# Optimization experiments

Hardware: AMD Instinct MI355X
Metric: run time of the kernel (lower is better)

Reference implementation:

```python
import jax, jax.numpy as jnp
import numpy as np

ALPHA = 0.2  # LeakyReLU negative slope
NEG_INF = -9e15


def setup_inputs() -> dict:
    key = jax.random.key(0)
    k1, k2, k3, k4, k5 = jax.random.split(key, 5)
    B, N, D = 4, 4096, 256
    feat = jax.random.normal(k1, (B, N, D), dtype=jnp.float32)
    adj = jax.random.randint(k2, (B, N, N), 0, 2, dtype=jnp.int32)
    W = jax.random.normal(k3, (D, D), dtype=jnp.float32) * (1.414 / np.sqrt(D))
    a_1 = jax.random.normal(k4, (D, 1), dtype=jnp.float32) * 0.1
    a_2 = jax.random.normal(k5, (D, 1), dtype=jnp.float32) * 0.1
    return {"feat": feat, "adj": adj, "W": W, "a_1": a_1, "a_2": a_2}


def reference(feat, adj, W, a_1, a_2):
    # h: [B, N, D]
    h = jnp.matmul(feat, W)
    Ax = jnp.matmul(h, a_1)  # [B, N, 1]
    Ay = jnp.matmul(h, a_2)  # [B, N, 1]
    # logits[b, i, j] = Ax[b, j] + Ay[b, i]
    logits = jnp.swapaxes(Ax, 1, 2) + Ay  # [B, N, N]
    e = jax.nn.leaky_relu(logits, negative_slope=ALPHA)
    e = jnp.where(adj > 0, e, jnp.float32(NEG_INF))
    attention = jax.nn.softmax(e, axis=-1)  # dropout p=0.0 -> identity
    h_prime = jnp.matmul(attention, feat)  # [B, N, in_features]
    h_out = jnp.matmul(h_prime, W)  # [B, N, out_features]
    return jax.nn.elu(h_out)
```

## Files before the change

### kernel.cpp

```cpp
#include <hip/hip_runtime.h>

typedef __attribute__((ext_vector_type(8))) short short8;
typedef __attribute__((ext_vector_type(4))) float f32x4;

#define LOG2E 1.44269504f

__device__ __forceinline__ short f2bf(float f) {
  unsigned u = __builtin_bit_cast(unsigned, f);
  u += 0x7fffu + ((u >> 16) & 1u);
  return (short)(u >> 16);
}

__global__ void gat_wvec(const float* __restrict__ W, const float* __restrict__ a1,
                         const float* __restrict__ a2, float* __restrict__ w1,
                         float* __restrict__ w2) {
  __shared__ float a1f[256], a2f[256];
  const int tid = threadIdx.x;
  a1f[tid] = a1[tid];
  a2f[tid] = a2[tid];
  __syncthreads();
  float s1 = 0.f, s2 = 0.f;
  const float4* wr = (const float4*)(W + (size_t)tid * 256);
  for (int d0 = 0; d0 < 64; ++d0) {
    float4 v = wr[d0];
    s1 += v.x * a1f[d0 * 4] + v.y * a1f[d0 * 4 + 1] + v.z * a1f[d0 * 4 + 2] + v.w * a1f[d0 * 4 + 3];
    s2 += v.x * a2f[d0 * 4] + v.y * a2f[d0 * 4 + 1] + v.z * a2f[d0 * 4 + 2] + v.w * a2f[d0 * 4 + 3];
  }
  w1[tid] = s1;
  w2[tid] = s2;
}

__global__ void convT(const float* __restrict__ src, short* __restrict__ dst,
                      int R, int C) {
  __shared__ short T[64][72];
  const int tid = threadIdx.x;
  const int bc = blockIdx.x, br = blockIdx.y, bb = blockIdx.z;
  const float* s = src + (size_t)bb * R * C;
  short* d = dst + (size_t)bb * R * C;
  const int rr = tid >> 2, cc = (tid & 3) << 4;
  const float4* sp = (const float4*)(s + (size_t)(br * 64 + rr) * C + bc * 64 + cc);
  alignas(16) short v[16];
#pragma unroll
  for (int g = 0; g < 4; ++g) {
    float4 x = sp[g];
    v[g * 4 + 0] = f2bf(x.x);
    v[g * 4 + 1] = f2bf(x.y);
    v[g * 4 + 2] = f2bf(x.z);
    v[g * 4 + 3] = f2bf(x.w);
  }
  *(short8*)&T[rr][cc] = *(short8*)&v[0];
  *(short8*)&T[rr][cc + 8] = *(short8*)&v[8];
  __syncthreads();
#pragma unroll
  for (int j = 0; j < 16; ++j) v[j] = T[cc + j][rr];
  short8* dp = (short8*)(d + (size_t)(bc * 64 + rr) * R + br * 64 + cc);
  dp[0] = *(short8*)&v[0];
  dp[1] = *(short8*)&v[8];
}

__global__ void gat_axay(const float* __restrict__ feat, const float* __restrict__ w1,
                         const float* __restrict__ w2, float* __restrict__ Ax,
                         float* __restrict__ Ay) {
  const int lane = threadIdx.x & 63;
  const int row = blockIdx.x * 4 + (threadIdx.x >> 6);
  float4 fv = *(const float4*)(feat + (size_t)row * 256 + lane * 4);
  const float4 w1v = *(const float4*)(w1 + lane * 4);
  const float4 w2v = *(const float4*)(w2 + lane * 4);
  float s1 = fv.x * w1v.x + fv.y * w1v.y + fv.z * w1v.z + fv.w * w1v.w;
  float s2 = fv.x * w2v.x + fv.y * w2v.y + fv.z * w2v.z + fv.w * w2v.w;
#pragma unroll
  for (int off = 32; off >= 1; off >>= 1) {
    s1 += __shfl_xor(s1, off);
    s2 += __shfl_xor(s2, off);
  }
  if (lane == 0) { Ax[row] = s1; Ay[row] = s2; }
}

__global__ void gat_max(const float* __restrict__ Ax, float* __restrict__ Mb) {
  __shared__ float red[256];
  const int b = blockIdx.x, tid = threadIdx.x;
  float m = -3.4e38f;
  for (int i = tid; i < 4096; i += 256) m = fmaxf(m, Ax[b * 4096 + i]);
  red[tid] = m;
  __syncthreads();
  for (int s = 128; s > 0; s >>= 1) {
    if (tid < s) red[tid] = fmaxf(red[tid], red[tid + s]);
    __syncthreads();
  }
  if (tid == 0) Mb[b] = red[0];
}

__global__ __launch_bounds__(256, 2) void gat_attn(
    const short* __restrict__ featT,
    const int* __restrict__ adj,
    const float* __restrict__ Ax, const float* __restrict__ Ay,
    const float* __restrict__ Mb,
    float* __restrict__ Opart,
    float* __restrict__ lpart)
{
  __shared__ short Pbuf[2][64][72];
  __shared__ float lsbuf[256];
  const int tid = threadIdx.x;
  const int blk = blockIdx.x;
  const int s = blk & 1;
  const int it = (blk >> 1) & 63;
  const int b = blk >> 7;
  const int i0 = it << 6;
  const int jbase = s << 11;

  const int r = tid >> 2;
  const int c0 = (tid & 3) << 4;

  const float ay = Ay[b * 4096 + i0 + r];
  float mr = ay + Mb[b];
  mr = mr > 0.f ? mr : 0.2f * mr;

  const int lane = tid & 63;
  const int w = tid >> 6;
  const int n0 = w << 6;
  const int l15 = lane & 15;
  const int q = lane >> 4;

  f32x4 acc[4][4];
#pragma unroll
  for (int i = 0; i < 4; ++i)
#pragma unroll
    for (int j = 0; j < 4; ++j) acc[i][j] = (f32x4){0.f, 0.f, 0.f, 0.f};

  float lsum = 0.f;

  const int4* adjp = (const int4*)(adj + ((size_t)(b * 4096 + i0 + r)) * 4096 + jbase + c0);
  const float4* axp = (const float4*)(Ax + b * 4096 + jbase + c0);
  const short* ftb = featT + ((size_t)(b * 256 + n0 + l15)) * 4096 + jbase + q * 8;

  int4 adv[4];
  float4 axv[4];
#pragma unroll
  for (int g = 0; g < 4; ++g) { adv[g] = adjp[g]; axv[g] = axp[g]; }

  for (int c = 0; c < 32; ++c) {
    alignas(16) short pk[16];
#pragma unroll
    for (int g = 0; g < 4; ++g) {
      const int* ai = (const int*)&adv[g];
      const float* af = (const float*)&axv[g];
#pragma unroll
      for (int u = 0; u < 4; ++u) {
        float lg = af[u] + ay;
        float e = lg > 0.f ? lg : 0.2f * lg;
        e = ai[u] > 0 ? e : -9e15f;
        float p = __builtin_amdgcn_exp2f((e - mr) * LOG2E);
        lsum += p;
        pk[g * 4 + u] = f2bf(p);
      }
    }
    {
      short8* dst = (short8*)&Pbuf[c & 1][r][c0];
      dst[0] = *(short8*)&pk[0];
      dst[1] = *(short8*)&pk[8];
    }
    __syncthreads();

    if (c < 31) {
#pragma unroll
      for (int g = 0; g < 4; ++g) {
        adv[g] = adjp[(c + 1) * 16 + g];
        axv[g] = axp[(c + 1) * 16 + g];
      }
    }

    const int j0 = c << 6;
#pragma unroll
    for (int k0 = 0; k0 < 64; k0 += 32) {
      short8 afr[4];
#pragma unroll
      for (int rt = 0; rt < 4; ++rt)
        afr[rt] = *(const short8*)&Pbuf[c & 1][rt * 16 + l15][k0 + q * 8];
#pragma unroll
      for (int ct = 0; ct < 4; ++ct) {
        short8 bfr = *(const short8*)(ftb + (size_t)ct * 16 * 4096 + j0 + k0);
#pragma unroll
        for (int rt = 0; rt < 4; ++rt)
          acc[rt][ct] = __builtin_amdgcn_mfma_f32_16x16x32_bf16(afr[rt], bfr, acc[rt][ct], 0, 0, 0);
      }
    }
  }

  lsbuf[tid] = lsum;
  __syncthreads();
  if (tid < 64) {
    float t = lsbuf[tid * 4] + lsbuf[tid * 4 + 1] + lsbuf[tid * 4 + 2] + lsbuf[tid * 4 + 3];
    lpart[(size_t)s * 16384 + b * 4096 + i0 + tid] = t;
  }
  float* Od = Opart + (size_t)s * 16384 * 256;
#pragma unroll
  for (int rt = 0; rt < 4; ++rt)
#pragma unroll
    for (int reg = 0; reg < 4; ++reg) {
      int row = i0 + rt * 16 + q * 4 + reg;
      float* orow = Od + ((size_t)(b * 4096 + row)) * 256 + n0 + l15;
#pragma unroll
      for (int ct = 0; ct < 4; ++ct) orow[ct * 16] = acc[rt][ct][reg];
    }
}

__global__ __launch_bounds__(256, 2) void gat_out(
    const float* __restrict__ O,
    const float* __restrict__ lp,
    const short* __restrict__ WT,
    float* __restrict__ out)
{
  const int tid = threadIdx.x;
  const int lane = tid & 63;
  const int w = tid >> 6;
  const int r0 = blockIdx.x << 6;
  const int n0 = w << 6;
  const int l15 = lane & 15;
  const int q = lane >> 4;

  f32x4 acc[4][4];
#pragma unroll
  for (int i = 0; i < 4; ++i)
#pragma unroll
    for (int j = 0; j < 4; ++j) acc[i][j] = (f32x4){0.f, 0.f, 0.f, 0.f};

  float linv[4];
#pragma unroll
  for (int rt = 0; rt < 4; ++rt) {
    int row = r0 + rt * 16 + l15;
    float l = lp[row] + lp[16384 + row];
    linv[rt] = l > 0.f ? 1.f / l : 0.f;
  }
  const float* O2 = O + (size_t)16384 * 256;

#pragma unroll 2
  for (int k0 = 0; k0 < 256; k0 += 32) {
    short8 afr[4];
#pragma unroll
    for (int rt = 0; rt < 4; ++rt) {
      size_t off = (size_t)(r0 + rt * 16 + l15) * 256 + k0 + q * 8;
      f32x4 h0 = *(const f32x4*)(O + off) + *(const f32x4*)(O2 + off);
      f32x4 h1 = *(const f32x4*)(O + off + 4) + *(const f32x4*)(O2 + off + 4);
      h0 *= linv[rt];
      h1 *= linv[rt];
      alignas(16) short p[8];
#pragma unroll
      for (int j = 0; j < 4; ++j) { p[j] = f2bf(h0[j]); p[4 + j] = f2bf(h1[j]); }
      afr[rt] = *(short8*)p;
    }
#pragma unroll
    for (int ct = 0; ct < 4; ++ct) {
      short8 bfr = *(const short8*)(WT + (size_t)(n0 + ct * 16 + l15) * 256 + k0 + q * 8);
#pragma unroll
      for (int rt = 0; rt < 4; ++rt)
        acc[rt][ct] = __builtin_amdgcn_mfma_f32_16x16x32_bf16(afr[rt], bfr, acc[rt][ct], 0, 0, 0);
    }
  }
#pragma unroll
  for (int rt = 0; rt < 4; ++rt)
#pragma unroll
    for (int reg = 0; reg < 4; ++reg) {
      int row = r0 + rt * 16 + q * 4 + reg;
#pragma unroll
      for (int ct = 0; ct < 4; ++ct) {
        float v = acc[rt][ct][reg];
        float o = v > 0.f ? v : (__builtin_amdgcn_exp2f(v * LOG2E) - 1.f);
        out[(size_t)row * 256 + n0 + ct * 16 + l15] = o;
      }
    }
}

extern "C" void kernel_launch(void* const* d_in, const int* in_sizes, int n_in,
                              void* d_out, int out_size, void* d_ws, size_t ws_size,
                              hipStream_t stream) {
  (void)in_sizes; (void)n_in; (void)out_size; (void)ws_size;
  const float* feat = (const float*)d_in[0];
  const int* adj = (const int*)d_in[1];
  const float* W = (const float*)d_in[2];
  const float* a1 = (const float*)d_in[3];
  const float* a2 = (const float*)d_in[4];
  float* out = (float*)d_out;

  char* ws = (char*)d_ws;
  short* featT = (short*)ws;
  float* Opart = (float*)(ws + 8388608);
  short* WT    = (short*)(ws + 41943040);
  float* w1    = (float*)(ws + 42074112);
  float* w2    = (float*)(ws + 42075136);
  float* Ax    = (float*)(ws + 42076160);
  float* Ay    = (float*)(ws + 42141696);
  float* lpart = (float*)(ws + 42207232);
  float* Mb    = (float*)(ws + 42338304);

  hipLaunchKernelGGL(gat_wvec, dim3(1), dim3(256), 0, stream, W, a1, a2, w1, w2);
  hipLaunchKernelGGL(convT, dim3(4, 4, 1), dim3(256), 0, stream, W, WT, 256, 256);
  hipLaunchKernelGGL(convT, dim3(4, 64, 4), dim3(256), 0, stream, feat, featT, 4096, 256);
  hipLaunchKernelGGL(gat_axay, dim3(4096), dim3(256), 0, stream, feat, w1, w2, Ax, Ay);
  hipLaunchKernelGGL(gat_max, dim3(4), dim3(256), 0, stream, Ax, Mb);
  hipLaunchKernelGGL(gat_attn, dim3(512), dim3(256), 0, stream, featT, adj, Ax, Ay, Mb, Opart, lpart);
  hipLaunchKernelGGL(gat_out, dim3(256), dim3(256), 0, stream, Opart, lpart, WT, out);
}
```

Measured before the change: 484.8 us.

## Fuse output projection into attention kernel and drop split-K over columns

```diff
diff --git a/kernel.cpp b/kernel.cpp
--- a/kernel.cpp
+++ b/kernel.cpp
@@ -2,6 +2,7 @@
 
 typedef __attribute__((ext_vector_type(8))) short short8;
 typedef __attribute__((ext_vector_type(4))) float f32x4;
+typedef __attribute__((ext_vector_type(4))) int i32x4;
 
 #define LOG2E 1.44269504f
 
@@ -95,21 +96,22 @@
     const int* __restrict__ adj,
     const float* __restrict__ Ax, const float* __restrict__ Ay,
     const float* __restrict__ Mb,
-    float* __restrict__ Opart,
-    float* __restrict__ lpart)
+    const short* __restrict__ WT,
+    float* __restrict__ out)
 {
-  __shared__ short Pbuf[2][64][72];
-  __shared__ float lsbuf[256];
+  __shared__ short Pbuf[2][32][72];
+  __shared__ short hbuf[32 * 264];
+  __shared__ float linv_s[32];
+
   const int tid = threadIdx.x;
   const int blk = blockIdx.x;
-  const int s = blk & 1;
-  const int it = (blk >> 1) & 63;
-  const int b = blk >> 7;
-  const int i0 = it << 6;
-  const int jbase = s << 11;
-
-  const int r = tid >> 2;
-  const int c0 = (tid & 3) << 4;
+  const int x = blk & 7;
+  const int b = x >> 1;
+  const int it = ((blk >> 3) << 1) | (x & 1);
+  const int i0 = it << 5;
+
+  const int r = tid >> 3;
+  const int c0 = (tid & 7) << 3;
 
   const float ay = Ay[b * 4096 + i0 + r];
   float mr = ay + Mb[b];
@@ -121,151 +123,111 @@
   const int l15 = lane & 15;
   const int q = lane >> 4;
 
-  f32x4 acc[4][4];
-#pragma unroll
-  for (int i = 0; i < 4; ++i)
+  f32x4 acc[2][4];
+#pragma unroll
+  for (int i = 0; i < 2; ++i)
 #pragma unroll
     for (int j = 0; j < 4; ++j) acc[i][j] = (f32x4){0.f, 0.f, 0.f, 0.f};
 
   float lsum = 0.f;
 
-  const int4* adjp = (const int4*)(adj + ((size_t)(b * 4096 + i0 + r)) * 4096 + jbase + c0);
-  const float4* axp = (const float4*)(Ax + b * 4096 + jbase + c0);
-  const short* ftb = featT + ((size_t)(b * 256 + n0 + l15)) * 4096 + jbase + q * 8;
-
-  int4 adv[4];
-  float4 axv[4];
-#pragma unroll
-  for (int g = 0; g < 4; ++g) { adv[g] = adjp[g]; axv[g] = axp[g]; }
-
-  for (int c = 0; c < 32; ++c) {
-    alignas(16) short pk[16];
-#pragma unroll
-    for (int g = 0; g < 4; ++g) {
-      const int* ai = (const int*)&adv[g];
+  const i32x4* adjp = (const i32x4*)(adj + ((size_t)(b * 4096 + i0 + r)) * 4096 + c0);
+  const float4* axp = (const float4*)(Ax + b * 4096 + c0);
+  const short* ftb = featT + ((size_t)(b * 256 + n0 + l15)) * 4096 + q * 8;
+
+  i32x4 adv[2];
+  float4 axv[2];
+  adv[0] = __builtin_nontemporal_load(adjp);
+  adv[1] = __builtin_nontemporal_load(adjp + 1);
+  axv[0] = axp[0];
+  axv[1] = axp[1];
+
+  for (int jc = 0; jc < 64; ++jc) {
+    alignas(16) short pk[8];
+#pragma unroll
+    for (int g = 0; g < 2; ++g) {
       const float* af = (const float*)&axv[g];
 #pragma unroll
       for (int u = 0; u < 4; ++u) {
         float lg = af[u] + ay;
         float e = lg > 0.f ? lg : 0.2f * lg;
-        e = ai[u] > 0 ? e : -9e15f;
+        e = adv[g][u] > 0 ? e : -9e15f;
         float p = __builtin_amdgcn_exp2f((e - mr) * LOG2E);
         lsum += p;
         pk[g * 4 + u] = f2bf(p);
       }
     }
-    {
-      short8* dst = (short8*)&Pbuf[c & 1][r][c0];
-      dst[0] = *(short8*)&pk[0];
-      dst[1] = *(short8*)&pk[8];
-    }
+    *(short8*)&Pbuf[jc & 1][r][c0] = *(short8*)pk;
     __syncthreads();
 
-    if (c < 31) {
-#pragma unroll
-      for (int g = 0; g < 4; ++g) {
-        adv[g] = adjp[(c + 1) * 16 + g];
-        axv[g] = axp[(c + 1) * 16 + g];
-      }
-    }
-
-    const int j0 = c << 6;
+    if (jc < 63) {
+      adv[0] = __builtin_nontemporal_load(adjp + (jc + 1) * 16);
+      adv[1] = __builtin_nontemporal_load(adjp + (jc + 1) * 16 + 1);
+      axv[0] = axp[(jc + 1) * 16];
+      axv[1] = axp[(jc + 1) * 16 + 1];
+    }
+
+    const int j0 = jc << 6;
 #pragma unroll
     for (int k0 = 0; k0 < 64; k0 += 32) {
-      short8 afr[4];
-#pragma unroll
-      for (int rt = 0; rt < 4; ++rt)
-        afr[rt] = *(const short8*)&Pbuf[c & 1][rt * 16 + l15][k0 + q * 8];
+      short8 afr0 = *(const short8*)&Pbuf[jc & 1][l15][k0 + q * 8];
+      short8 afr1 = *(const short8*)&Pbuf[jc & 1][16 + l15][k0 + q * 8];
 #pragma unroll
       for (int ct = 0; ct < 4; ++ct) {
         short8 bfr = *(const short8*)(ftb + (size_t)ct * 16 * 4096 + j0 + k0);
-#pragma unroll
-        for (int rt = 0; rt < 4; ++rt)
-          acc[rt][ct] = __builtin_amdgcn_mfma_f32_16x16x32_bf16(afr[rt], bfr, acc[rt][ct], 0, 0, 0);
+        acc[0][ct] = __builtin_amdgcn_mfma_f32_16x16x32_bf16(afr0, bfr, acc[0][ct], 0, 0, 0);
+        acc[1][ct] = __builtin_amdgcn_mfma_f32_16x16x32_bf16(afr1, bfr, acc[1][ct], 0, 0, 0);
       }
     }
   }
 
-  lsbuf[tid] = lsum;
-  __syncthreads();
-  if (tid < 64) {
-    float t = lsbuf[tid * 4] + lsbuf[tid * 4 + 1] + lsbuf[tid * 4 + 2] + lsbuf[tid * 4 + 3];
-    lpart[(size_t)s * 16384 + b * 4096 + i0 + tid] = t;
-  }
-  float* Od = Opart + (size_t)s * 16384 * 256;
-#pragma unroll
-  for (int rt = 0; rt < 4; ++rt)
+  float s = lsum;
+  s += __shfl_xor(s, 1);
+  s += __shfl_xor(s, 2);
+  s += __shfl_xor(s, 4);
+  if ((tid & 7) == 0) linv_s[r] = s > 0.f ? 1.f / s : 0.f;
+  __syncthreads();
+
+#pragma unroll
+  for (int rt = 0; rt < 2; ++rt)
+#pragma unroll
+    for (int reg = 0; reg < 4; ++reg) {
+      int lr = rt * 16 + q * 4 + reg;
+      float li = linv_s[lr];
+#pragma unroll
+      for (int ct = 0; ct < 4; ++ct)
+        hbuf[lr * 264 + n0 + ct * 16 + l15] = f2bf(acc[rt][ct][reg] * li);
+    }
+  __syncthreads();
+
+#pragma unroll
+  for (int i = 0; i < 2; ++i)
+#pragma unroll
+    for (int j = 0; j < 4; ++j) acc[i][j] = (f32x4){0.f, 0.f, 0.f, 0.f};
+
+#pragma unroll 2
+  for (int k0 = 0; k0 < 256; k0 += 32) {
+    short8 afr0 = *(const short8*)&hbuf[l15 * 264 + k0 + q * 8];
+    short8 afr1 = *(const short8*)&hbuf[(16 + l15) * 264 + k0 + q * 8];
+#pragma unroll
+    for (int ct = 0; ct < 4; ++ct) {
+      short8 bfr = *(const short8*)(WT + (size_t)(n0 + ct * 16 + l15) * 256 + k0 + q * 8);
+      acc[0][ct] = __builtin_amdgcn_mfma_f32_16x16x32_bf16(afr0, bfr, acc[0][ct], 0, 0, 0);
+      acc[1][ct] = __builtin_amdgcn_mfma_f32_16x16x32_bf16(afr1, bfr, acc[1][ct], 0, 0, 0);
+    }
+  }
+
+#pragma unroll
+  for (int rt = 0; rt < 2; ++rt)
 #pragma unroll
     for (int reg = 0; reg < 4; ++reg) {
       int row = i0 + rt * 16 + q * 4 + reg;
-      float* orow = Od + ((size_t)(b * 4096 + row)) * 256 + n0 + l15;
-#pragma unroll
-      for (int ct = 0; ct < 4; ++ct) orow[ct * 16] = acc[rt][ct][reg];
-    }
-}
-
-__global__ __launch_bounds__(256, 2) void gat_out(
-    const float* __restrict__ O,
-    const float* __restrict__ lp,
-    const short* __restrict__ WT,
-    float* __restrict__ out)
-{
-  const int tid = threadIdx.x;
-  const int lane = tid & 63;
-  const int w = tid >> 6;
-  const int r0 = blockIdx.x << 6;
-  const int n0 = w << 6;
-  const int l15 = lane & 15;
-  const int q = lane >> 4;
-
-  f32x4 acc[4][4];
-#pragma unroll
-  for (int i = 0; i < 4; ++i)
-#pragma unroll
-    for (int j = 0; j < 4; ++j) acc[i][j] = (f32x4){0.f, 0.f, 0.f, 0.f};
-
-  float linv[4];
-#pragma unroll
-  for (int rt = 0; rt < 4; ++rt) {
-    int row = r0 + rt * 16 + l15;
-    float l = lp[row] + lp[16384 + row];
-    linv[rt] = l > 0.f ? 1.f / l : 0.f;
-  }
-  const float* O2 = O + (size_t)16384 * 256;
-
-#pragma unroll 2
-  for (int k0 = 0; k0 < 256; k0 += 32) {
-    short8 afr[4];
-#pragma unroll
-    for (int rt = 0; rt < 4; ++rt) {
-      size_t off = (size_t)(r0 + rt * 16 + l15) * 256 + k0 + q * 8;
-      f32x4 h0 = *(const f32x4*)(O + off) + *(const f32x4*)(O2 + off);
-      f32x4 h1 = *(const f32x4*)(O + off + 4) + *(const f32x4*)(O2 + off + 4);
-      h0 *= linv[rt];
-      h1 *= linv[rt];
-      alignas(16) short p[8];
-#pragma unroll
-      for (int j = 0; j < 4; ++j) { p[j] = f2bf(h0[j]); p[4 + j] = f2bf(h1[j]); }
-      afr[rt] = *(short8*)p;
-    }
-#pragma unroll
-    for (int ct = 0; ct < 4; ++ct) {
-      short8 bfr = *(const short8*)(WT + (size_t)(n0 + ct * 16 + l15) * 256 + k0 + q * 8);
-#pragma unroll
-      for (int rt = 0; rt < 4; ++rt)
-        acc[rt][ct] = __builtin_amdgcn_mfma_f32_16x16x32_bf16(afr[rt], bfr, acc[rt][ct], 0, 0, 0);
-    }
-  }
-#pragma unroll
-  for (int rt = 0; rt < 4; ++rt)
-#pragma unroll
-    for (int reg = 0; reg < 4; ++reg) {
-      int row = r0 + rt * 16 + q * 4 + reg;
+      float* orow = out + ((size_t)(b * 4096 + row)) * 256 + n0 + l15;
 #pragma unroll
       for (int ct = 0; ct < 4; ++ct) {
         float v = acc[rt][ct][reg];
         float o = v > 0.f ? v : (__builtin_amdgcn_exp2f(v * LOG2E) - 1.f);
-        out[(size_t)row * 256 + n0 + ct * 16 + l15] = o;
+        __builtin_nontemporal_store(o, orow + ct * 16);
       }
     }
 }
@@ -283,20 +245,17 @@
 
   char* ws = (char*)d_ws;
   short* featT = (short*)ws;
-  float* Opart = (float*)(ws + 8388608);
-  short* WT    = (short*)(ws + 41943040);
-  float* w1    = (float*)(ws + 42074112);
-  float* w2    = (float*)(ws + 42075136);
-  float* Ax    = (float*)(ws + 42076160);
-  float* Ay    = (float*)(ws + 42141696);
-  float* lpart = (float*)(ws + 42207232);
-  float* Mb    = (float*)(ws + 42338304);
+  short* WT    = (short*)(ws + 8388608);
+  float* w1    = (float*)(ws + 8519680);
+  float* w2    = (float*)(ws + 8520704);
+  float* Ax    = (float*)(ws + 8521728);
+  float* Ay    = (float*)(ws + 8587264);
+  float* Mb    = (float*)(ws + 8652800);
 
   hipLaunchKernelGGL(gat_wvec, dim3(1), dim3(256), 0, stream, W, a1, a2, w1, w2);
   hipLaunchKernelGGL(convT, dim3(4, 4, 1), dim3(256), 0, stream, W, WT, 256, 256);
   hipLaunchKernelGGL(convT, dim3(4, 64, 4), dim3(256), 0, stream, feat, featT, 4096, 256);
   hipLaunchKernelGGL(gat_axay, dim3(4096), dim3(256), 0, stream, feat, w1, w2, Ax, Ay);
   hipLaunchKernelGGL(gat_max, dim3(4), dim3(256), 0, stream, Ax, Mb);
-  hipLaunchKernelGGL(gat_attn, dim3(512), dim3(256), 0, stream, featT, adj, Ax, Ay, Mb, Opart, lpart);
-  hipLaunchKernelGGL(gat_out, dim3(256), dim3(256), 0, stream, Opart, lpart, WT, out);
-}
+  hipLaunchKernelGGL(gat_attn, dim3(512), dim3(256), 0, stream, featT, adj, Ax, Ay, Mb, WT, out);
+}
```

Result: slower. 515.7 us (+6.4%).
